# Optimization experiments

Measured on AMD Instinct MI355X. Metric: run time of the kernel, lower is better.

## Reference

```python
import jax, jax.numpy as jnp
import numpy as np

B = 2048
E = 128      # embedding_dim
H = 1024     # hidden_dim
V = 100000   # num_products
C = 5000     # num_categories
U = 50000    # num_urls
LAG = 5
N_SCALAR = 16
CAT_SIZES = np.array([7, 24, 2, 4, 2, 2, 2])  # dayofweek, hour, weekend, product_action_id, price_null, description_null, img_null
CAT_OFFSETS = np.concatenate([[0], np.cumsum(CAT_SIZES)[:-1]])
N_SMALL = int(CAT_SIZES.sum())  # 41
IGNORE_INDEX = 0  # low_targets
EPS = 1e-5


def setup_inputs() -> dict:
    key = jax.random.key(0)
    ks = jax.random.split(key, 40)
    i = iter(range(40))
    nrm = lambda shape, s=0.01: jax.random.normal(ks[next(i)], shape, dtype=jnp.float32) * s
    inp = {}
    # forward inputs
    inp['scalar_feats'] = jax.random.normal(ks[next(i)], (B, N_SCALAR), dtype=jnp.float32)
    inp['lag_descriptions'] = jax.random.normal(ks[next(i)], (B, 8), dtype=jnp.float32)
    inp['lag_imgs'] = jax.random.normal(ks[next(i)], (B, 8), dtype=jnp.float32)
    inp['lag_products'] = jax.random.randint(ks[next(i)], (B, LAG), 0, V)
    inp['first_product'] = jax.random.randint(ks[next(i)], (B, 1), 0, V)
    inp['lag_categories'] = jax.random.randint(ks[next(i)], (B, LAG), 0, C)
    inp['first_category'] = jax.random.randint(ks[next(i)], (B, 1), 0, C)
    inp['lag_urls'] = jax.random.randint(ks[next(i)], (B, LAG), 0, U)
    inp['first_url'] = jax.random.randint(ks[next(i)], (B, 1), 0, U)
    raw = jax.random.randint(ks[next(i)], (B, 7), 0, 1 << 16)
    inp['cat_feats'] = raw % jnp.asarray(CAT_SIZES)[None, :]
    inp['target'] = jax.random.randint(ks[next(i)], (B,), 0, V)
    # parameters
    inp['emb_products'] = nrm((V, E))
    inp['emb_categories'] = nrm((C, E))
    inp['emb_urls'] = nrm((U, E))
    inp['emb_small'] = nrm((N_SMALL, E))
    inp['W_scalar'] = nrm((N_SCALAR, E), 0.1)  # nn.Linear(1, E, bias=False) weights, stacked
    inp['g_scalar'] = jnp.ones((N_SCALAR, E), jnp.float32)
    inp['b_scalar'] = jnp.zeros((N_SCALAR, E), jnp.float32)
    inp['W_desc'] = nrm((E, 8), 0.1)
    inp['g_desc'] = jnp.ones((E,), jnp.float32)
    inp['b_desc'] = jnp.zeros((E,), jnp.float32)
    inp['W_imgs'] = nrm((E, 8), 0.1)
    inp['g_imgs'] = jnp.ones((E,), jnp.float32)
    inp['b_imgs'] = jnp.zeros((E,), jnp.float32)
    D_in = (3 * LAG + 1) * E  # 2048
    inp['W1'] = nrm((H, D_in), 0.02); inp['b1'] = jnp.zeros((H,), jnp.float32)
    inp['g1'] = jnp.ones((H,), jnp.float32); inp['be1'] = jnp.zeros((H,), jnp.float32)
    inp['p1'] = jnp.full((1,), 0.25, jnp.float32)
    inp['W2'] = nrm((H, H), 0.02); inp['b2'] = jnp.zeros((H,), jnp.float32)
    inp['g2'] = jnp.ones((H,), jnp.float32); inp['be2'] = jnp.zeros((H,), jnp.float32)
    inp['p2'] = jnp.full((1,), 0.25, jnp.float32)
    inp['W3'] = nrm((E, H), 0.02); inp['b3'] = jnp.zeros((E,), jnp.float32)
    inp['g3'] = jnp.ones((E,), jnp.float32); inp['be3'] = jnp.zeros((E,), jnp.float32)
    inp['p3'] = jnp.full((1,), 0.25, jnp.float32)
    inp['out_bias'] = nrm((V,))
    return inp


def _bn(x, g, b):
    # training-mode BatchNorm1d: batch statistics over axis 0, biased variance
    m = x.mean(0)
    v = x.var(0)
    return (x - m) * jax.lax.rsqrt(v + EPS) * g + b


def _prelu(x, p):
    return jnp.where(x > 0, x, p * x)


def reference(scalar_feats, lag_descriptions, lag_imgs, emb_products, emb_categories,
              emb_urls, emb_small, W_scalar, g_scalar, b_scalar, W_desc, g_desc, b_desc,
              W_imgs, g_imgs, b_imgs, W1, b1, g1, be1, p1, W2, b2, g2, be2, p2,
              W3, b3, g3, be3, p3, out_bias,
              lag_products, first_product, lag_categories, first_category,
              lag_urls, first_url, cat_feats, target):
    b = scalar_feats.shape[0]
    # gather branches
    lag_embed = emb_products[lag_products].reshape(b, -1)        # [B, 5E]
    category_embed = emb_categories[lag_categories].reshape(b, -1)
    url_embed = emb_urls[lag_urls].reshape(b, -1)
    x = (emb_products[first_product[:, 0]]
         + emb_categories[first_category[:, 0]]
         + emb_urls[first_url[:, 0]])                            # [B, E]
    # 7 small categorical embeddings packed into one table
    idx = cat_feats + jnp.asarray(CAT_OFFSETS)[None, :]
    x = x + emb_small[idx].sum(axis=1)
    # 16 scalar linear->BN->ReLU branches, vectorized over the branch axis
    y = scalar_feats[:, :, None] * W_scalar[None, :, :]          # [B, 16, E]
    x = x + jax.nn.relu(_bn(y, g_scalar, b_scalar)).sum(axis=1)
    # 8-wide linear->BN->ReLU branches
    x = x + jax.nn.relu(_bn(lag_descriptions @ W_desc.T, g_desc, b_desc))
    x = x + jax.nn.relu(_bn(lag_imgs @ W_imgs.T, g_imgs, b_imgs))
    # concat + 3-layer MLP (dropout = identity in eval)
    h = jnp.concatenate([lag_embed, category_embed, url_embed, x], axis=-1)  # [B, 16E]
    h = _prelu(_bn(h @ W1.T + b1, g1, be1), p1)
    h = _prelu(_bn(h @ W2.T + b2, g2, be2), p2)
    h = _prelu(_bn(h @ W3.T + b3, g3, be3), p3)                  # [B, E]
    # tied-weight output layer
    logits = h @ emb_products.T + out_bias                        # [B, V]
    # cross-entropy with ignore_index
    lp = jax.nn.log_softmax(logits, axis=-1)
    nll = -jnp.take_along_axis(lp, target[:, None], axis=-1)[:, 0]
    mask = (target != IGNORE_INDEX).astype(logits.dtype)
    loss = (nll * mask).sum() / mask.sum()
    return logits, loss
```

## Files before the change

### kernel.cpp

```cpp
#include <hip/hip_runtime.h>
#include <math.h>

static constexpr int BATCH = 2048;
static constexpr int E     = 128;
static constexpr int HDIM  = 1024;
static constexpr int V     = 100000;
static constexpr int VPAD  = 100096;
static constexpr int NCT   = 782;
static constexpr int DIN   = 2048;
static constexpr float EPS = 1e-5f;

static constexpr int O_SSUM = 0;
static constexpr int O_SSQ  = 16;
static constexpr int O_ZDS  = 32;
static constexpr int O_ZDQ  = 160;
static constexpr int O_ZIS  = 288;
static constexpr int O_ZIQ  = 416;
static constexpr int O_H1S  = 544;
static constexpr int O_H2S  = 2592;
static constexpr int O_H3S  = 4640;

static constexpr size_t OFF_STATS = 0;
static constexpr size_t OFF_H0   = 32768;
static constexpr size_t OFF_W1B  = OFF_H0   + 8388608;
static constexpr size_t OFF_W2B  = OFF_W1B  + 4194304;
static constexpr size_t OFF_W3B  = OFF_W2B  + 2097152;
static constexpr size_t OFF_EPB  = OFF_W3B  + 262144;
static constexpr size_t OFF_H1F  = OFF_EPB  + 25624576;
static constexpr size_t OFF_H1N  = OFF_H1F  + 8388608;
static constexpr size_t OFF_H2F  = OFF_H1N  + 4194304;
static constexpr size_t OFF_H2N  = OFF_H2F  + 8388608;
static constexpr size_t OFF_H3F  = OFF_H2N  + 4194304;
static constexpr size_t OFF_H3N  = OFF_H3F  + 1048576;
static constexpr size_t OFF_PMAX = OFF_H3N  + 524288;
static constexpr size_t OFF_PSUM = OFF_PMAX + 6406144;
static constexpr size_t OFF_LSE  = OFF_PSUM + 6406144;

typedef __bf16 bf16x8 __attribute__((ext_vector_type(8)));
typedef float  f32x4  __attribute__((ext_vector_type(4)));

__device__ __forceinline__ unsigned short f2bf(float f) {
    unsigned int u = __builtin_bit_cast(unsigned int, f);
    u += 0x7FFFu + ((u >> 16) & 1u);
    return (unsigned short)(u >> 16);
}

__global__ __launch_bounds__(256) void cvt_bf16(const float* __restrict__ s,
                                                unsigned short* __restrict__ d, int n4) {
    int i = blockIdx.x * 256 + threadIdx.x;
    int stride = gridDim.x * 256;
    for (; i < n4; i += stride) {
        float4 v = ((const float4*)s)[i];
        ushort4 o;
        o.x = f2bf(v.x); o.y = f2bf(v.y); o.z = f2bf(v.z); o.w = f2bf(v.w);
        ((ushort4*)d)[i] = o;
    }
}

__global__ __launch_bounds__(256) void stats1(const float* __restrict__ sf,
                                              const float* __restrict__ ldsc,
                                              const float* __restrict__ limg,
                                              const float* __restrict__ Wd,
                                              const float* __restrict__ Wi,
                                              float* __restrict__ stats) {
    __shared__ float redA[256], redB[256];
    const int t = threadIdx.x;
    const int r0 = blockIdx.x * 128;
    {
        int c = t & 15, rg = t >> 4;
        float s = 0.f, s2 = 0.f;
        for (int i = 0; i < 8; i++) {
            float v = sf[(size_t)(r0 + rg * 8 + i) * 16 + c];
            s += v; s2 += v * v;
        }
        redA[rg * 16 + c] = s; redB[rg * 16 + c] = s2;
        __syncthreads();
        if (t < 16) {
            float S = 0.f, Q = 0.f;
            for (int g = 0; g < 16; g++) { S += redA[g * 16 + t]; Q += redB[g * 16 + t]; }
            atomicAdd(&stats[O_SSUM + t], S);
            atomicAdd(&stats[O_SSQ + t], Q);
        }
        __syncthreads();
    }
    for (int br = 0; br < 2; br++) {
        const float* X = br ? limg : ldsc;
        const float* W = br ? Wi : Wd;
        int e = t & 127, rg = t >> 7;
        float wreg[8];
        #pragma unroll
        for (int k = 0; k < 8; k++) wreg[k] = W[e * 8 + k];
        float s = 0.f, s2 = 0.f;
        for (int i = 0; i < 64; i++) {
            int r = r0 + rg + 2 * i;
            float z = 0.f;
            #pragma unroll
            for (int k = 0; k < 8; k++) z += X[(size_t)r * 8 + k] * wreg[k];
            s += z; s2 += z * z;
        }
        redA[rg * 128 + e] = s; redB[rg * 128 + e] = s2;
        __syncthreads();
        if (t < 128) {
            int base = br ? O_ZIS : O_ZDS;
            atomicAdd(&stats[base + t], redA[t] + redA[128 + t]);
            atomicAdd(&stats[base + 128 + t], redB[t] + redB[128 + t]);
        }
        __syncthreads();
    }
}

__global__ __launch_bounds__(128) void build_h0_k(
    const float* __restrict__ sf, const float* __restrict__ ldsc, const float* __restrict__ limg,
    const int* __restrict__ lp, const int* __restrict__ fp, const int* __restrict__ lc,
    const int* __restrict__ fc, const int* __restrict__ lu, const int* __restrict__ fu,
    const int* __restrict__ cat,
    const float* __restrict__ eP, const float* __restrict__ eC, const float* __restrict__ eU,
    const float* __restrict__ eS,
    const float* __restrict__ Wsc, const float* __restrict__ gsc, const float* __restrict__ bsc,
    const float* __restrict__ Wd, const float* __restrict__ gd, const float* __restrict__ bd,
    const float* __restrict__ Wi, const float* __restrict__ gi, const float* __restrict__ bi,
    const float* __restrict__ stats, unsigned short* __restrict__ h0) {
    const int b = blockIdx.x, e = threadIdx.x;
    unsigned short* out = h0 + (size_t)b * DIN;
    #pragma unroll
    for (int j = 0; j < 5; j++) out[j * 128 + e] = f2bf(eP[(size_t)lp[b * 5 + j] * 128 + e]);
    #pragma unroll
    for (int j = 0; j < 5; j++) out[(5 + j) * 128 + e] = f2bf(eC[(size_t)lc[b * 5 + j] * 128 + e]);
    #pragma unroll
    for (int j = 0; j < 5; j++) out[(10 + j) * 128 + e] = f2bf(eU[(size_t)lu[b * 5 + j] * 128 + e]);
    float x = eP[(size_t)fp[b] * 128 + e] + eC[(size_t)fc[b] * 128 + e] + eU[(size_t)fu[b] * 128 + e];
    const int offs[7] = {0, 7, 31, 33, 37, 39, 41};
    #pragma unroll
    for (int j = 0; j < 7; j++) x += eS[(size_t)(offs[j] + cat[b * 7 + j]) * 128 + e];
    const float invB = 1.f / 2048.f;
    #pragma unroll
    for (int i = 0; i < 16; i++) {
        float ms = stats[O_SSUM + i] * invB;
        float vs = stats[O_SSQ + i] * invB - ms * ms;
        float wv = Wsc[i * 128 + e];
        float val = (sf[b * 16 + i] - ms) * wv * rsqrtf(vs * wv * wv + EPS) * gsc[i * 128 + e] + bsc[i * 128 + e];
        x += fmaxf(val, 0.f);
    }
    {
        float z = 0.f;
        #pragma unroll
        for (int k = 0; k < 8; k++) z += ldsc[b * 8 + k] * Wd[e * 8 + k];
        float md = stats[O_ZDS + e] * invB;
        float vd = stats[O_ZDQ + e] * invB - md * md;
        x += fmaxf((z - md) * rsqrtf(vd + EPS) * gd[e] + bd[e], 0.f);
    }
    {
        float z = 0.f;
        #pragma unroll
        for (int k = 0; k < 8; k++) z += limg[b * 8 + k] * Wi[e * 8 + k];
        float mi = stats[O_ZIS + e] * invB;
        float vi = stats[O_ZIQ + e] * invB - mi * mi;
        x += fmaxf((z - mi) * rsqrtf(vi + EPS) * gi[e] + bi[e], 0.f);
    }
    out[15 * 128 + e] = f2bf(x);
}

template <int BM, int BN, int MODE>
__global__ __launch_bounds__(256) void gemm_bt(
    const unsigned short* __restrict__ A, int lda,
    const unsigned short* __restrict__ Bm, int ldb,
    const float* __restrict__ bias,
    float* __restrict__ C, int ldc, int K,
    float* __restrict__ pmax, float* __restrict__ psum) {
    constexpr int WM = BM / 2, WN = BN / 2, TI = WM / 16, TJ = WN / 16;
    __shared__ uint4 sA[BM * 4];
    __shared__ uint4 sB[BN * 4];
    const int t = threadIdx.x;
    const int w = t >> 6, lane = t & 63;
    const int wr = w >> 1, wc = w & 1;
    const int m16 = lane & 15, q = lane >> 4;
    const int m0 = blockIdx.y * BM, n0 = blockIdx.x * BN;

    f32x4 acc[TI][TJ];
    #pragma unroll
    for (int i = 0; i < TI; i++)
        #pragma unroll
        for (int j = 0; j < TJ; j++) acc[i][j] = (f32x4){0.f, 0.f, 0.f, 0.f};

    for (int k0 = 0; k0 < K; k0 += 32) {
        __syncthreads();
        for (int c = t; c < (BM + BN) * 4; c += 256) {
            int isB = c >= BM * 4;
            int cc = isB ? c - BM * 4 : c;
            int row = cc >> 2, kc = cc & 3;
            const unsigned short* src = isB ? (Bm + (size_t)(n0 + row) * ldb + k0)
                                            : (A + (size_t)(m0 + row) * lda + k0);
            uint4 v = ((const uint4*)src)[kc];
            int pos = row * 4 + (kc ^ ((row >> 1) & 3));
            (isB ? sB : sA)[pos] = v;
        }
        __syncthreads();
        bf16x8 aF[TI], bF[TJ];
        #pragma unroll
        for (int i = 0; i < TI; i++) {
            int row = wr * WM + i * 16 + m16;
            aF[i] = ((const bf16x8*)sA)[row * 4 + (q ^ ((row >> 1) & 3))];
        }
        #pragma unroll
        for (int j = 0; j < TJ; j++) {
            int row = wc * WN + j * 16 + m16;
            bF[j] = ((const bf16x8*)sB)[row * 4 + (q ^ ((row >> 1) & 3))];
        }
        #pragma unroll
        for (int i = 0; i < TI; i++)
            #pragma unroll
            for (int j = 0; j < TJ; j++)
                acc[i][j] = __builtin_amdgcn_mfma_f32_16x16x32_bf16(aF[i], bF[j], acc[i][j], 0, 0, 0);
    }

    if constexpr (MODE == 0) {
        #pragma unroll
        for (int j = 0; j < TJ; j++) {
            int col = n0 + wc * WN + j * 16 + m16;
            float bv = bias[col];
            #pragma unroll
            for (int i = 0; i < TI; i++)
                #pragma unroll
                for (int r = 0; r < 4; r++) {
                    int row = m0 + wr * WM + i * 16 + q * 4 + r;
                    C[(size_t)row * ldc + col] = acc[i][j][r] + bv;
                }
        }
    } else {
        float bias_j[TJ];
        bool val_j[TJ];
        int colbase = n0 + wc * WN;
        #pragma unroll
        for (int j = 0; j < TJ; j++) {
            int col = colbase + j * 16 + m16;
            val_j[j] = (col < V);
            bias_j[j] = val_j[j] ? bias[col] : 0.f;
        }
        __syncthreads();
        float* srmax = (float*)sA;
        float* srsum = srmax + BM * 2;
        float* sM    = srsum + BM * 2;
        #pragma unroll
        for (int i = 0; i < TI; i++)
            #pragma unroll
            for (int r = 0; r < 4; r++) {
                int rowb = wr * WM + i * 16 + q * 4 + r;
                float mx = -INFINITY;
                #pragma unroll
                for (int j = 0; j < TJ; j++)
                    if (val_j[j]) mx = fmaxf(mx, acc[i][j][r] + bias_j[j]);
                #pragma unroll
                for (int msk = 1; msk < 16; msk <<= 1) mx = fmaxf(mx, __shfl_xor(mx, msk, 64));
                if (m16 == 0) srmax[rowb * 2 + wc] = mx;
            }
        __syncthreads();
        if (t < BM) sM[t] = fmaxf(srmax[t * 2], srmax[t * 2 + 1]);
        __syncthreads();
        #pragma unroll
        for (int i = 0; i < TI; i++)
            #pragma unroll
            for (int r = 0; r < 4; r++) {
                int rowb = wr * WM + i * 16 + q * 4 + r;
                int grow = m0 + rowb;
                float Mr = sM[rowb];
                float sm = 0.f;
                #pragma unroll
                for (int j = 0; j < TJ; j++) {
                    if (val_j[j]) {
                        float v = acc[i][j][r] + bias_j[j];
                        C[(size_t)grow * ldc + colbase + j * 16 + m16] = v;
                        sm += __expf(v - Mr);
                    }
                }
                #pragma unroll
                for (int msk = 1; msk < 16; msk <<= 1) sm += __shfl_xor(sm, msk, 64);
                if (m16 == 0) srsum[rowb * 2 + wc] = sm;
            }
        __syncthreads();
        if (t < BM) {
            pmax[(size_t)blockIdx.x * BATCH + m0 + t] = sM[t];
            psum[(size_t)blockIdx.x * BATCH + m0 + t] = srsum[t * 2] + srsum[t * 2 + 1];
        }
    }
}

__global__ __launch_bounds__(256) void colstats(const float* __restrict__ X,
                                                float* __restrict__ sums, int N) {
    int c = threadIdx.x & 63, rg = threadIdx.x >> 6;
    int col = blockIdx.x * 64 + c;
    int r0 = blockIdx.y * 128 + rg * 32;
    float s = 0.f, s2 = 0.f;
    for (int i = 0; i < 32; i++) {
        float v = X[(size_t)(r0 + i) * N + col];
        s += v; s2 += v * v;
    }
    __shared__ float rs[4][64], rq[4][64];
    rs[rg][c] = s; rq[rg][c] = s2;
    __syncthreads();
    if (threadIdx.x < 64) {
        float S = 0.f, Q = 0.f;
        for (int g = 0; g < 4; g++) { S += rs[g][threadIdx.x]; Q += rq[g][threadIdx.x]; }
        atomicAdd(&sums[col], S);
        atomicAdd(&sums[N + col], Q);
    }
}

__global__ __launch_bounds__(256) void bn_prelu(const float* __restrict__ X,
                                                unsigned short* __restrict__ Y,
                                                const float* __restrict__ sums,
                                                const float* __restrict__ g,
                                                const float* __restrict__ be,
                                                const float* __restrict__ p, int N, int total4) {
    int i = blockIdx.x * 256 + threadIdx.x;
    if (i >= total4) return;
    float pv = p[0];
    int n4 = N >> 2;
    int c4 = i % n4;
    float4 v = ((const float4*)X)[i];
    float vv[4] = {v.x, v.y, v.z, v.w};
    unsigned short oo[4];
    #pragma unroll
    for (int k = 0; k < 4; k++) {
        int n = c4 * 4 + k;
        float m = sums[n] * (1.f / 2048.f);
        float var = sums[N + n] * (1.f / 2048.f) - m * m;
        float val = (vv[k] - m) * rsqrtf(var + EPS) * g[n] + be[n];
        val = val > 0.f ? val : pv * val;
        oo[k] = f2bf(val);
    }
    ushort4 o; o.x = oo[0]; o.y = oo[1]; o.z = oo[2]; o.w = oo[3];
    ((ushort4*)Y)[i] = o;
}

__global__ __launch_bounds__(256) void lse_k(const float* __restrict__ pmax,
                                             const float* __restrict__ psum,
                                             float* __restrict__ lse, int ntiles) {
    int r = blockIdx.x * 256 + threadIdx.x;
    if (r >= BATCH) return;
    float m = -INFINITY, s = 0.f;
    for (int t = 0; t < ntiles; t++) {
        float pm = pmax[(size_t)t * BATCH + r];
        float ps = psum[(size_t)t * BATCH + r];
        if (pm > m) { s = s * __expf(m - pm) + ps; m = pm; }
        else        { s += ps * __expf(pm - m); }
    }
    lse[r] = m + __logf(s);
}

__global__ __launch_bounds__(256) void loss_k(const float* __restrict__ logits,
                                              const float* __restrict__ lse,
                                              const int* __restrict__ target,
                                              float* __restrict__ out_loss) {
    int t = threadIdx.x;
    float s = 0.f, c = 0.f;
    for (int r = t; r < BATCH; r += 256) {
        int tg = target[r];
        if (tg != 0) {
            s += lse[r] - logits[(size_t)r * V + tg];
            c += 1.f;
        }
    }
    #pragma unroll
    for (int m = 1; m < 64; m <<= 1) { s += __shfl_xor(s, m, 64); c += __shfl_xor(c, m, 64); }
    __shared__ float ss[4], sc[4];
    if ((t & 63) == 0) { ss[t >> 6] = s; sc[t >> 6] = c; }
    __syncthreads();
    if (t == 0) {
        float S = ss[0] + ss[1] + ss[2] + ss[3];
        float C = sc[0] + sc[1] + sc[2] + sc[3];
        out_loss[0] = S / C;
    }
}

extern "C" void kernel_launch(void* const* d_in, const int* in_sizes, int n_in,
                              void* d_out, int out_size, void* d_ws, size_t ws_size,
                              hipStream_t stream) {
    const float* sf   = (const float*)d_in[0];
    const float* ldsc = (const float*)d_in[1];
    const float* limg = (const float*)d_in[2];
    const int* lp  = (const int*)d_in[3];
    const int* fp  = (const int*)d_in[4];
    const int* lc  = (const int*)d_in[5];
    const int* fc  = (const int*)d_in[6];
    const int* lu  = (const int*)d_in[7];
    const int* fu  = (const int*)d_in[8];
    const int* cat = (const int*)d_in[9];
    const int* tgt = (const int*)d_in[10];
    const float* eP  = (const float*)d_in[11];
    const float* eC  = (const float*)d_in[12];
    const float* eU  = (const float*)d_in[13];
    const float* eS  = (const float*)d_in[14];
    const float* Wsc = (const float*)d_in[15];
    const float* gsc = (const float*)d_in[16];
    const float* bsc = (const float*)d_in[17];
    const float* Wd  = (const float*)d_in[18];
    const float* gd  = (const float*)d_in[19];
    const float* bd  = (const float*)d_in[20];
    const float* Wi  = (const float*)d_in[21];
    const float* gi  = (const float*)d_in[22];
    const float* bi  = (const float*)d_in[23];
    const float* W1  = (const float*)d_in[24];
    const float* b1  = (const float*)d_in[25];
    const float* g1  = (const float*)d_in[26];
    const float* be1 = (const float*)d_in[27];
    const float* p1  = (const float*)d_in[28];
    const float* W2  = (const float*)d_in[29];
    const float* b2  = (const float*)d_in[30];
    const float* g2  = (const float*)d_in[31];
    const float* be2 = (const float*)d_in[32];
    const float* p2  = (const float*)d_in[33];
    const float* W3  = (const float*)d_in[34];
    const float* b3  = (const float*)d_in[35];
    const float* g3  = (const float*)d_in[36];
    const float* be3 = (const float*)d_in[37];
    const float* p3  = (const float*)d_in[38];
    const float* ob  = (const float*)d_in[39];

    char* w = (char*)d_ws;
    float* stats = (float*)(w + OFF_STATS);
    unsigned short* h0  = (unsigned short*)(w + OFF_H0);
    unsigned short* W1b = (unsigned short*)(w + OFF_W1B);
    unsigned short* W2b = (unsigned short*)(w + OFF_W2B);
    unsigned short* W3b = (unsigned short*)(w + OFF_W3B);
    unsigned short* ePb = (unsigned short*)(w + OFF_EPB);
    float* h1f = (float*)(w + OFF_H1F);
    unsigned short* h1n = (unsigned short*)(w + OFF_H1N);
    float* h2f = (float*)(w + OFF_H2F);
    unsigned short* h2n = (unsigned short*)(w + OFF_H2N);
    float* h3f = (float*)(w + OFF_H3F);
    unsigned short* h3n = (unsigned short*)(w + OFF_H3N);
    float* pmaxb = (float*)(w + OFF_PMAX);
    float* psumb = (float*)(w + OFF_PSUM);
    float* lseb  = (float*)(w + OFF_LSE);
    float* logits = (float*)d_out;

    hipMemsetAsync(stats, 0, 32768, stream);

    cvt_bf16<<<512, 256, 0, stream>>>(W1, W1b, (HDIM * DIN) / 4);
    cvt_bf16<<<512, 256, 0, stream>>>(W2, W2b, (HDIM * HDIM) / 4);
    cvt_bf16<<<128, 256, 0, stream>>>(W3, W3b, (E * HDIM) / 4);
    cvt_bf16<<<1024, 256, 0, stream>>>(eP, ePb, (V * E) / 4);

    stats1<<<16, 256, 0, stream>>>(sf, ldsc, limg, Wd, Wi, stats);

    build_h0_k<<<BATCH, 128, 0, stream>>>(sf, ldsc, limg, lp, fp, lc, fc, lu, fu, cat,
                                          eP, eC, eU, eS, Wsc, gsc, bsc, Wd, gd, bd,
                                          Wi, gi, bi, stats, h0);

    gemm_bt<128, 64, 0><<<dim3(HDIM / 64, BATCH / 128), 256, 0, stream>>>(
        h0, DIN, W1b, DIN, b1, h1f, HDIM, DIN, nullptr, nullptr);
    colstats<<<dim3(HDIM / 64, 16), 256, 0, stream>>>(h1f, stats + O_H1S, HDIM);
    bn_prelu<<<(BATCH * HDIM / 4) / 256, 256, 0, stream>>>(h1f, h1n, stats + O_H1S, g1, be1, p1,
                                                           HDIM, BATCH * HDIM / 4);

    gemm_bt<128, 64, 0><<<dim3(HDIM / 64, BATCH / 128), 256, 0, stream>>>(
        h1n, HDIM, W2b, HDIM, b2, h2f, HDIM, HDIM, nullptr, nullptr);
    colstats<<<dim3(HDIM / 64, 16), 256, 0, stream>>>(h2f, stats + O_H2S, HDIM);
    bn_prelu<<<(BATCH * HDIM / 4) / 256, 256, 0, stream>>>(h2f, h2n, stats + O_H2S, g2, be2, p2,
                                                           HDIM, BATCH * HDIM / 4);

    gemm_bt<64, 32, 0><<<dim3(E / 32, BATCH / 64), 256, 0, stream>>>(
        h2n, HDIM, W3b, HDIM, b3, h3f, E, HDIM, nullptr, nullptr);
    colstats<<<dim3(E / 64, 16), 256, 0, stream>>>(h3f, stats + O_H3S, E);
    bn_prelu<<<(BATCH * E / 4) / 256, 256, 0, stream>>>(h3f, h3n, stats + O_H3S, g3, be3, p3,
                                                        E, BATCH * E / 4);

    gemm_bt<128, 128, 1><<<dim3(NCT, BATCH / 128), 256, 0, stream>>>(
        h3n, E, ePb, E, ob, logits, V, E, pmaxb, psumb);

    lse_k<<<BATCH / 256, 256, 0, stream>>>(pmaxb, psumb, lseb, NCT);
    loss_k<<<1, 256, 0, stream>>>(logits, lseb, tgt, logits + (size_t)BATCH * V);
}
```

Baseline: 1.662 ms.

## Fuse embedding bf16 conversion into dedicated logits kernel with resident B tile

```diff
diff --git a/kernel.cpp b/kernel.cpp
--- a/kernel.cpp
+++ b/kernel.cpp
@@ -5,7 +5,6 @@
 static constexpr int E     = 128;
 static constexpr int HDIM  = 1024;
 static constexpr int V     = 100000;
-static constexpr int VPAD  = 100096;
 static constexpr int NCT   = 782;
 static constexpr int DIN   = 2048;
 static constexpr float EPS = 1e-5f;
@@ -65,12 +64,12 @@
                                               float* __restrict__ stats) {
     __shared__ float redA[256], redB[256];
     const int t = threadIdx.x;
-    const int r0 = blockIdx.x * 128;
+    const int r0 = blockIdx.x * 32;
     {
         int c = t & 15, rg = t >> 4;
         float s = 0.f, s2 = 0.f;
-        for (int i = 0; i < 8; i++) {
-            float v = sf[(size_t)(r0 + rg * 8 + i) * 16 + c];
+        for (int i = 0; i < 2; i++) {
+            float v = sf[(size_t)(r0 + rg * 2 + i) * 16 + c];
             s += v; s2 += v * v;
         }
         redA[rg * 16 + c] = s; redB[rg * 16 + c] = s2;
@@ -91,7 +90,7 @@
         #pragma unroll
         for (int k = 0; k < 8; k++) wreg[k] = W[e * 8 + k];
         float s = 0.f, s2 = 0.f;
-        for (int i = 0; i < 64; i++) {
+        for (int i = 0; i < 16; i++) {
             int r = r0 + rg + 2 * i;
             float z = 0.f;
             #pragma unroll
@@ -213,74 +212,152 @@
                 acc[i][j] = __builtin_amdgcn_mfma_f32_16x16x32_bf16(aF[i], bF[j], acc[i][j], 0, 0, 0);
     }
 
-    if constexpr (MODE == 0) {
-        #pragma unroll
-        for (int j = 0; j < TJ; j++) {
-            int col = n0 + wc * WN + j * 16 + m16;
-            float bv = bias[col];
-            #pragma unroll
-            for (int i = 0; i < TI; i++)
+    #pragma unroll
+    for (int j = 0; j < TJ; j++) {
+        int col = n0 + wc * WN + j * 16 + m16;
+        float bv = bias[col];
+        #pragma unroll
+        for (int i = 0; i < TI; i++)
+            #pragma unroll
+            for (int r = 0; r < 4; r++) {
+                int row = m0 + wr * WM + i * 16 + q * 4 + r;
+                C[(size_t)row * ldc + col] = acc[i][j][r] + bv;
+            }
+    }
+}
+
+__global__ __launch_bounds__(256, 2) void logits_k(
+    const unsigned short* __restrict__ A,
+    const float* __restrict__ eP,
+    const float* __restrict__ bias,
+    float* __restrict__ C,
+    float* __restrict__ pmax, float* __restrict__ psum) {
+    __shared__ uint4 sB[2048];
+    __shared__ uint4 sA[2048];
+    __shared__ float sred[640];
+    float* srmax = sred;
+    float* srsum = sred + 256;
+    float* sM    = sred + 512;
+
+    const int t = threadIdx.x;
+    const int w = t >> 6, lane = t & 63;
+    const int wr = w >> 1, wc = w & 1;
+    const int m16 = lane & 15, q = lane >> 4;
+    const int n0 = blockIdx.x * 128;
+    const int mbase = blockIdx.y * 1024;
+
+    uint4 av[8];
+    #pragma unroll
+    for (int i = 0; i < 8; i++) {
+        int c = i * 256 + t, row = c >> 4, ch = c & 15;
+        av[i] = ((const uint4*)(A + (size_t)(mbase + row) * 128))[ch ^ (row & 7)];
+    }
+    #pragma unroll
+    for (int i = 0; i < 8; i++) {
+        int c = i * 256 + t, row = c >> 4, ch = c & 15;
+        int gc = n0 + row, sc = ch ^ (row & 7);
+        uint4 v = {0u, 0u, 0u, 0u};
+        if (gc < V) {
+            const float4* p = (const float4*)(eP + (size_t)gc * 128 + sc * 8);
+            float4 f0 = p[0], f1 = p[1];
+            v.x = (unsigned)f2bf(f0.x) | ((unsigned)f2bf(f0.y) << 16);
+            v.y = (unsigned)f2bf(f0.z) | ((unsigned)f2bf(f0.w) << 16);
+            v.z = (unsigned)f2bf(f1.x) | ((unsigned)f2bf(f1.y) << 16);
+            v.w = (unsigned)f2bf(f1.z) | ((unsigned)f2bf(f1.w) << 16);
+        }
+        sB[row * 16 + ch] = v;
+    }
+    #pragma unroll
+    for (int i = 0; i < 8; i++) sA[i * 256 + t] = av[i];
+
+    float bias_j[4]; bool val_j[4];
+    const int colbase = n0 + wc * 64;
+    #pragma unroll
+    for (int j = 0; j < 4; j++) {
+        int col = colbase + j * 16 + m16;
+        val_j[j] = (col < V);
+        bias_j[j] = val_j[j] ? bias[col] : 0.f;
+    }
+    __syncthreads();
+
+    for (int mt = 0; mt < 8; ++mt) {
+        const int m0 = mbase + mt * 128;
+        f32x4 acc[4][4];
+        #pragma unroll
+        for (int i = 0; i < 4; i++)
+            #pragma unroll
+            for (int j = 0; j < 4; j++) acc[i][j] = (f32x4){0.f, 0.f, 0.f, 0.f};
+        #pragma unroll
+        for (int kk = 0; kk < 4; kk++) {
+            bf16x8 aF[4], bF[4];
+            #pragma unroll
+            for (int i = 0; i < 4; i++) {
+                int row = wr * 64 + i * 16 + m16;
+                aF[i] = ((const bf16x8*)sA)[row * 16 + ((kk * 4 + q) ^ (row & 7))];
+            }
+            #pragma unroll
+            for (int j = 0; j < 4; j++) {
+                int row = wc * 64 + j * 16 + m16;
+                bF[j] = ((const bf16x8*)sB)[row * 16 + ((kk * 4 + q) ^ (row & 7))];
+            }
+            #pragma unroll
+            for (int i = 0; i < 4; i++)
                 #pragma unroll
-                for (int r = 0; r < 4; r++) {
-                    int row = m0 + wr * WM + i * 16 + q * 4 + r;
-                    C[(size_t)row * ldc + col] = acc[i][j][r] + bv;
-                }
-        }
-    } else {
-        float bias_j[TJ];
-        bool val_j[TJ];
-        int colbase = n0 + wc * WN;
-        #pragma unroll
-        for (int j = 0; j < TJ; j++) {
-            int col = colbase + j * 16 + m16;
-            val_j[j] = (col < V);
-            bias_j[j] = val_j[j] ? bias[col] : 0.f;
-        }
-        __syncthreads();
-        float* srmax = (float*)sA;
-        float* srsum = srmax + BM * 2;
-        float* sM    = srsum + BM * 2;
-        #pragma unroll
-        for (int i = 0; i < TI; i++)
+                for (int j = 0; j < 4; j++)
+                    acc[i][j] = __builtin_amdgcn_mfma_f32_16x16x32_bf16(aF[i], bF[j], acc[i][j], 0, 0, 0);
+        }
+        #pragma unroll
+        for (int i = 0; i < 4; i++)
             #pragma unroll
             for (int r = 0; r < 4; r++) {
-                int rowb = wr * WM + i * 16 + q * 4 + r;
+                int rowb = wr * 64 + i * 16 + q * 4 + r;
                 float mx = -INFINITY;
                 #pragma unroll
-                for (int j = 0; j < TJ; j++)
+                for (int j = 0; j < 4; j++)
                     if (val_j[j]) mx = fmaxf(mx, acc[i][j][r] + bias_j[j]);
                 #pragma unroll
                 for (int msk = 1; msk < 16; msk <<= 1) mx = fmaxf(mx, __shfl_xor(mx, msk, 64));
                 if (m16 == 0) srmax[rowb * 2 + wc] = mx;
             }
         __syncthreads();
-        if (t < BM) sM[t] = fmaxf(srmax[t * 2], srmax[t * 2 + 1]);
-        __syncthreads();
-        #pragma unroll
-        for (int i = 0; i < TI; i++)
+        if (t < 128) sM[t] = fmaxf(srmax[t * 2], srmax[t * 2 + 1]);
+        __syncthreads();
+        if (mt + 1 < 8) {
+            #pragma unroll
+            for (int i = 0; i < 8; i++) {
+                int c = i * 256 + t, row = c >> 4, ch = c & 15;
+                av[i] = ((const uint4*)(A + (size_t)(m0 + 128 + row) * 128))[ch ^ (row & 7)];
+            }
+        }
+        #pragma unroll
+        for (int i = 0; i < 4; i++)
             #pragma unroll
             for (int r = 0; r < 4; r++) {
-                int rowb = wr * WM + i * 16 + q * 4 + r;
+                int rowb = wr * 64 + i * 16 + q * 4 + r;
                 int grow = m0 + rowb;
                 float Mr = sM[rowb];
-                float sm = 0.f;
+                float sm_ = 0.f;
                 #pragma unroll
-                for (int j = 0; j < TJ; j++) {
+                for (int j = 0; j < 4; j++)
                     if (val_j[j]) {
                         float v = acc[i][j][r] + bias_j[j];
-                        C[(size_t)grow * ldc + colbase + j * 16 + m16] = v;
-                        sm += __expf(v - Mr);
+                        C[(size_t)grow * V + colbase + j * 16 + m16] = v;
+                        sm_ += __expf(v - Mr);
                     }
-                }
                 #pragma unroll
-                for (int msk = 1; msk < 16; msk <<= 1) sm += __shfl_xor(sm, msk, 64);
-                if (m16 == 0) srsum[rowb * 2 + wc] = sm;
+                for (int msk = 1; msk < 16; msk <<= 1) sm_ += __shfl_xor(sm_, msk, 64);
+                if (m16 == 0) srsum[rowb * 2 + wc] = sm_;
             }
         __syncthreads();
-        if (t < BM) {
+        if (t < 128) {
             pmax[(size_t)blockIdx.x * BATCH + m0 + t] = sM[t];
             psum[(size_t)blockIdx.x * BATCH + m0 + t] = srsum[t * 2] + srsum[t * 2 + 1];
         }
+        if (mt + 1 < 8) {
+            #pragma unroll
+            for (int i = 0; i < 8; i++) sA[i * 256 + t] = av[i];
+        }
+        __syncthreads();
     }
 }
 
@@ -335,16 +412,32 @@
 __global__ __launch_bounds__(256) void lse_k(const float* __restrict__ pmax,
                                              const float* __restrict__ psum,
                                              float* __restrict__ lse, int ntiles) {
-    int r = blockIdx.x * 256 + threadIdx.x;
-    if (r >= BATCH) return;
+    __shared__ float shm[4 * 64], shs[4 * 64];
+    int lr = threadIdx.x & 63;
+    int ch = threadIdx.x >> 6;
+    int r = blockIdx.x * 64 + lr;
+    int per = (ntiles + 3) >> 2;
+    int t0 = ch * per, t1 = t0 + per;
+    if (t1 > ntiles) t1 = ntiles;
     float m = -INFINITY, s = 0.f;
-    for (int t = 0; t < ntiles; t++) {
-        float pm = pmax[(size_t)t * BATCH + r];
-        float ps = psum[(size_t)t * BATCH + r];
+    for (int tt = t0; tt < t1; ++tt) {
+        float pm = pmax[(size_t)tt * BATCH + r];
+        float ps = psum[(size_t)tt * BATCH + r];
         if (pm > m) { s = s * __expf(m - pm) + ps; m = pm; }
         else        { s += ps * __expf(pm - m); }
     }
-    lse[r] = m + __logf(s);
+    shm[ch * 64 + lr] = m; shs[ch * 64 + lr] = s;
+    __syncthreads();
+    if (threadIdx.x < 64) {
+        float M = shm[lr], S = shs[lr];
+        #pragma unroll
+        for (int g = 1; g < 4; ++g) {
+            float pm = shm[g * 64 + lr], ps = shs[g * 64 + lr];
+            if (pm > M) { S = S * __expf(M - pm) + ps; M = pm; }
+            else        { S += ps * __expf(pm - M); }
+        }
+        lse[blockIdx.x * 64 + lr] = M + __logf(S);
+    }
 }
 
 __global__ __launch_bounds__(256) void loss_k(const float* __restrict__ logits,
@@ -422,7 +515,6 @@
     unsigned short* W1b = (unsigned short*)(w + OFF_W1B);
     unsigned short* W2b = (unsigned short*)(w + OFF_W2B);
     unsigned short* W3b = (unsigned short*)(w + OFF_W3B);
-    unsigned short* ePb = (unsigned short*)(w + OFF_EPB);
     float* h1f = (float*)(w + OFF_H1F);
     unsigned short* h1n = (unsigned short*)(w + OFF_H1N);
     float* h2f = (float*)(w + OFF_H2F);
@@ -439,9 +531,8 @@
     cvt_bf16<<<512, 256, 0, stream>>>(W1, W1b, (HDIM * DIN) / 4);
     cvt_bf16<<<512, 256, 0, stream>>>(W2, W2b, (HDIM * HDIM) / 4);
     cvt_bf16<<<128, 256, 0, stream>>>(W3, W3b, (E * HDIM) / 4);
-    cvt_bf16<<<1024, 256, 0, stream>>>(eP, ePb, (V * E) / 4);
-
-    stats1<<<16, 256, 0, stream>>>(sf, ldsc, limg, Wd, Wi, stats);
+
+    stats1<<<64, 256, 0, stream>>>(sf, ldsc, limg, Wd, Wi, stats);
 
     build_h0_k<<<BATCH, 128, 0, stream>>>(sf, ldsc, limg, lp, fp, lc, fc, lu, fu, cat,
                                           eP, eC, eU, eS, Wsc, gsc, bsc, Wd, gd, bd,
@@ -465,9 +556,8 @@
     bn_prelu<<<(BATCH * E / 4) / 256, 256, 0, stream>>>(h3f, h3n, stats + O_H3S, g3, be3, p3,
                                                         E, BATCH * E / 4);
 
-    gemm_bt<128, 128, 1><<<dim3(NCT, BATCH / 128), 256, 0, stream>>>(
-        h3n, E, ePb, E, ob, logits, V, E, pmaxb, psumb);
-
-    lse_k<<<BATCH / 256, 256, 0, stream>>>(pmaxb, psumb, lseb, NCT);
+    logits_k<<<dim3(NCT, 2), 256, 0, stream>>>(h3n, eP, ob, logits, pmaxb, psumb);
+
+    lse_k<<<BATCH / 64, 256, 0, stream>>>(pmaxb, psumb, lseb, NCT);
     loss_k<<<1, 256, 0, stream>>>(logits, lseb, tgt, logits + (size_t)BATCH * V);
 }
```

After: 1.450 ms. 12.8% less time.
